# Optimization experiments

Measured on AMD Instinct MI355X. Metric: run time of the kernel, lower is better.

The kernel has to match this reference:

```python
import jax, jax.numpy as jnp
import numpy as np

B, CIN, COUT, N, TIN = 8, 64, 64, 207, 54
K, NHID, SL, KT = 8, 64, 3, 3
HEADS, STRIDE, PL = 8, 4, 8
TIME_NUM, OUT_LEN = 120, 48
E = COUT * PL            # 512 = attention embed dim (embed_size*patch_len)
PD = E // HEADS          # 64 per-head dim
PNUM = (OUT_LEN + STRIDE - PL) // STRIDE + 1   # 12 patches
EPS = 1e-5


def setup_inputs():
    keys = iter(jax.random.split(jax.random.key(0), 48))
    def rn(shape, s):
        return jax.random.normal(next(keys), shape, jnp.float32) * s
    d = {}
    d['x'] = rn((B, CIN, N, TIN), 1.0)
    d['adj'] = jax.random.uniform(next(keys), (SL, N, N), jnp.float32) / N
    d['W_conv1'] = rn((COUT, CIN), 0.125); d['b_conv1'] = rn((COUT,), 0.02)
    d['g_T'] = jnp.ones((TIN,), jnp.float32); d['b_T'] = jnp.zeros((TIN,), jnp.float32)
    d['g_S'] = jnp.ones((N,), jnp.float32); d['b_S'] = jnp.zeros((N,), jnp.float32)
    d['W_time'] = rn((2*COUT, 3*COUT, 1, KT), 1.0/np.sqrt(3*COUT*KT)); d['b_time'] = rn((2*COUT,), 0.02)
    d['wq1'] = rn((SL, K, COUT, NHID), 0.125); d['wv1'] = rn((SL, K, COUT, NHID), 0.125)
    d['bias1'] = rn((SL, NHID), 0.05)
    d['wq2'] = rn((SL, K, NHID, 2*COUT), 0.125); d['wv2'] = rn((SL, K, NHID, 2*COUT), 0.125)
    d['bias2'] = rn((SL, 2*COUT), 0.05)
    d['W_mlp'] = rn((2*COUT, SL*2*COUT, 1, KT), 1.0/np.sqrt(SL*2*COUT*KT)); d['b_mlp'] = rn((2*COUT,), 0.02)
    d['emb_T'] = rn((TIME_NUM, E), 0.02)
    d['Wq'] = rn((PD, PD), 0.125); d['bq'] = rn((PD,), 0.02)
    d['Wk'] = rn((PD, PD), 0.125); d['bk'] = rn((PD,), 0.02)
    d['Wv'] = rn((PD, PD), 0.125); d['bv'] = rn((PD,), 0.02)
    d['W_fc'] = rn((E, E), 1.0/np.sqrt(E)); d['b_fc'] = rn((E,), 0.02)
    d['g1'] = jnp.ones((E,), jnp.float32); d['b1n'] = jnp.zeros((E,), jnp.float32)
    d['g2'] = jnp.ones((E,), jnp.float32); d['b2n'] = jnp.zeros((E,), jnp.float32)
    d['W_ff1'] = rn((E, 4*COUT), 1.0/np.sqrt(E)); d['b_ff1'] = rn((4*COUT,), 0.02)
    d['W_ff2'] = rn((4*COUT, E), 1.0/np.sqrt(4*COUT)); d['b_ff2'] = rn((E,), 0.02)
    d['W_rp'] = rn((PNUM*PL, OUT_LEN), 1.0/np.sqrt(PNUM*PL)); d['b_rp'] = rn((OUT_LEN,), 0.02)
    d['g_bn'] = jnp.ones((COUT,), jnp.float32); d['b_bn'] = jnp.zeros((COUT,), jnp.float32)
    return d


def _ln(v, g, b, axis):
    m = jnp.mean(v, axis=axis, keepdims=True)
    var = jnp.var(v, axis=axis, keepdims=True)
    xhat = (v - m) * jax.lax.rsqrt(var + EPS)
    shp = [1] * v.ndim; shp[axis] = -1
    return xhat * g.reshape(shp) + b.reshape(shp)


def _gconv(x, wq, wv, bias, a):
    # x: [B,C,N,L]; wq/wv: [K,C,D]; a: [N,N]  -- multi-basis sigmoid-gated GCN
    q = jnp.einsum('bcnl,kcd->kbdnl', x, wq)
    v = jnp.einsum('bcnl,kcd->kbdnl', x, wv)
    s = jnp.sum(jax.nn.sigmoid(q) * v, axis=0)           # [B,D,N,L]
    out = jnp.einsum('nk,bcnl->bckl', a, s)              # adjacency aggregation (exact index order of source)
    return out + bias[None, :, None, None]


def _conv2d(x, w, b, dil):
    y = jax.lax.conv_general_dilated(x, w, (1, 1), 'VALID', rhs_dilation=(1, dil),
                                     dimension_numbers=('NCHW', 'OIHW', 'NCHW'))
    return y + b[None, :, None, None]


def reference(x, adj, W_conv1, b_conv1, g_T, b_T, g_S, b_S, W_time, b_time,
              wq1, wv1, bias1, wq2, wv2, bias2, W_mlp, b_mlp, emb_T,
              Wq, bq, Wk, bk, Wv, bv, W_fc, b_fc, g1, b1n, g2, b2n,
              W_ff1, b_ff1, W_ff2, b_ff2, W_rp, b_rp, g_bn, b_bn):
    residual = jnp.einsum('oc,bcnl->bonl', W_conv1, x) + b_conv1[None, :, None, None]
    xcat = jnp.concatenate([residual, _ln(residual, g_T, b_T, 3), _ln(residual, g_S, b_S, 2)], axis=1)
    h = _conv2d(xcat, W_time, b_time, 2)                 # [B,2C,N,50]
    h = jnp.tanh(h[:, :COUT]) * jax.nn.sigmoid(h[:, COUT:])
    outs = [_gconv(jax.nn.relu(_gconv(h, wq1[i], wv1[i], bias1[i], adj[i])),
                   wq2[i], wv2[i], bias2[i], adj[i]) for i in range(SL)]
    g = _conv2d(jnp.concatenate(outs, axis=1), W_mlp, b_mlp, 1)   # [B,2C,N,48]
    g = jnp.tanh(g[:, :COUT]) * jax.nn.sigmoid(g[:, COUT:])      # [B,C,N,48]
    # --- TTransformer with patching ---
    z = jnp.pad(g, ((0, 0), (0, 0), (0, 0), (0, STRIDE)))        # pad time by stride (52 >= patch_len)
    idx = jnp.arange(PNUM)[:, None] * STRIDE + jnp.arange(PL)[None, :]
    patches = z[..., idx]                                        # [B,C,N,P,PL] unfold
    q0 = patches.reshape(B, N, PNUM, E)                          # row-major reshape, as in torch source
    xe = q0 + emb_T[:PNUM][None, None]
    qh = xe.reshape(B, N, PNUM, HEADS, PD)
    qs = qh @ Wq + bq; ks = qh @ Wk + bk; vs = qh @ Wv + bv
    scores = jnp.einsum('bnqhd,bnkhd->bnqkh', qs, ks)
    att = jax.nn.softmax(scores / jnp.sqrt(jnp.float32(E)), axis=2)   # softmax over QUERY axis (faithful to source)
    ao = jnp.einsum('bnqkh,bnkhd->bnqhd', att, vs).reshape(B, N, PNUM, E) @ W_fc + b_fc
    M = _ln(ao + xe, g1, b1n, 3)
    ff = jax.nn.relu(M @ W_ff1 + b_ff1) @ W_ff2 + b_ff2
    U = _ln(M + ff, g2, b2n, 3)
    o = (U + xe + M).reshape(B, N, COUT, PNUM * PL) @ W_rp + b_rp     # [B,N,C,48]
    o = jnp.transpose(o, (0, 2, 1, 3))                               # [B,C,N,48]
    # --- BatchNorm2d (training-mode batch stats) over residual sum ---
    y = o + residual[..., -OUT_LEN:]
    m = jnp.mean(y, axis=(0, 2, 3), keepdims=True)
    var = jnp.var(y, axis=(0, 2, 3), keepdims=True)
    return (y - m) * jax.lax.rsqrt(var + EPS) * g_bn[None, :, None, None] + b_bn[None, :, None, None]
```

## Files before the change

### kernel.cpp

```cpp
#include <hip/hip_runtime.h>
#include <hip/hip_bf16.h>

#define TPB 256
#define TPA 512

constexpr int Bx = 8, Cc = 64, Nn = 207, Tin = 54, Kb = 8;
constexpr int LP = 52, NP = Nn * LP;
constexpr int NPa = 10816;
constexpr int L50 = 50, Tout = 48;
constexpr int Ee = 512, Pn = 12;
constexpr float EPSF = 1e-5f;
constexpr int SRDF = 516;

constexpr size_t O_RESID = 0;
constexpr size_t O_LNTM  = O_RESID + (size_t)Bx*Cc*Nn*Tin;
constexpr size_t O_LNTR  = O_LNTM  + (size_t)Bx*Cc*Nn;
constexpr size_t O_LNSM  = O_LNTR  + (size_t)Bx*Cc*Nn;
constexpr size_t O_LNSR  = O_LNSM  + (size_t)Bx*Cc*Tin;
constexpr size_t O_XCAT  = O_LNSR  + (size_t)Bx*Cc*Tin;
constexpr size_t O_RB    = O_XCAT  + (size_t)Bx*192*Nn*Tin;
constexpr size_t O_H     = O_RB    + (size_t)Bx*128*NP;
constexpr size_t O_GACC  = O_H     + (size_t)Bx*64*NP;
constexpr size_t O_GG    = O_GACC  + (size_t)Bx*128*Nn*Tout;
constexpr size_t O_XE    = O_GG    + (size_t)Bx*64*Nn*Tout;
constexpr size_t O_WTT   = O_XE    + (size_t)Bx*Nn*Pn*Ee;
constexpr size_t O_WTM   = O_WTT   + (size_t)128*192*3;
constexpr size_t O_BNST  = O_WTM   + (size_t)128*384*3;
constexpr size_t O_WTB   = O_BNST + 128;
constexpr size_t O_ADJT  = O_WTB  + (size_t)128*576/2;
constexpr size_t O_HT    = O_H;
constexpr size_t O_WQ1B  = O_ADJT + (size_t)3*13*7*512/2;
constexpr size_t O_WV1B  = O_WQ1B + (size_t)24*4*2*512/2;
constexpr size_t O_WQ2B  = O_WV1B + (size_t)24*4*2*512/2;
constexpr size_t O_WV2B  = O_WQ2B + (size_t)24*8*2*512/2;
constexpr size_t O_WQT   = O_WV2B + (size_t)24*8*2*512/2;
constexpr size_t O_WKT   = O_WQT  + 2048;
constexpr size_t O_WVT   = O_WKT  + 2048;
constexpr size_t O_WFCT  = O_WVT  + 2048;
constexpr size_t O_WF1T  = O_WFCT + 131072;
constexpr size_t O_WF2T  = O_WF1T + 65536;

#define FMA4(acc, sA_, vB_) { (acc).x += (sA_)*(vB_).x; (acc).y += (sA_)*(vB_).y; (acc).z += (sA_)*(vB_).z; (acc).w += (sA_)*(vB_).w; }

typedef __attribute__((ext_vector_type(8))) short bf16x8;
typedef __attribute__((ext_vector_type(4))) float f32x4;

__device__ __forceinline__ float sigm(float x){ return 1.0f/(1.0f+__expf(-x)); }
__device__ __forceinline__ ushort f2bf(float x){ __hip_bfloat16 h = __float2bfloat16(x); return *(ushort*)&h; }

__global__ __launch_bounds__(TPB) void k_residual(const float* __restrict__ x, const float* __restrict__ W,
                                                  const float* __restrict__ bias, float* __restrict__ out,
                                                  float* __restrict__ lnm, float* __restrict__ lnr){
  int n = blockIdx.x, b = blockIdx.y;
  __shared__ __align__(16) float sX[Cc][Tin];
  __shared__ __align__(16) float sW[Cc*Cc];
  __shared__ __align__(16) float sO[Cc][Tin];
  int tid = threadIdx.x;
  for(int i=tid;i<Cc*Tin;i+=TPB){ int c=i/Tin, l=i%Tin; sX[c][l] = x[((size_t)(b*Cc+c)*Nn+n)*Tin+l]; }
  for(int i=tid;i<Cc*Cc;i+=TPB) sW[i]=W[i];
  __syncthreads();
  for(int i=tid;i<Cc*Tin;i+=TPB){
    int o=i/Tin, l=i%Tin; float acc=bias[o];
    #pragma unroll 8
    for(int c=0;c<Cc;c++) acc += sW[o*Cc+c]*sX[c][l];
    out[((size_t)(b*Cc+o)*Nn+n)*Tin+l]=acc;
    sO[o][l]=acc;
  }
  __syncthreads();
  if(tid < Cc){
    float s=0.f,s2=0.f;
    for(int l=0;l<Tin;l++){ float v=sO[tid][l]; s+=v; s2+=v*v; }
    float m=s*(1.f/Tin); float var=s2*(1.f/Tin)-m*m;
    int row = (b*Cc+tid)*Nn + n;
    lnm[row]=m; lnr[row]=rsqrtf(fmaxf(var,0.f)+EPSF);
  }
}

__global__ __launch_bounds__(TPB) void k_lnS(const float* __restrict__ r, float* __restrict__ mean, float* __restrict__ rstd){
  int row = blockIdx.x*TPB + threadIdx.x;
  if(row >= Bx*Cc*Tin) return;
  int l = row % Tin; int bc = row / Tin;
  const float* p = r + (size_t)bc*Nn*Tin + l;
  float s=0.f,s2=0.f;
  for(int n=0;n<Nn;n++){ float v=p[(size_t)n*Tin]; s+=v; s2+=v*v; }
  float m=s*(1.f/Nn); float var=s2*(1.f/Nn)-m*m;
  mean[row]=m; rstd[row]=rsqrtf(fmaxf(var,0.f)+EPSF);
}

struct WJob { const float* W; ushort* F; int K, N, KS, NT, sStride, total, type; };
struct WJobs { WJob j[14]; };

__global__ __launch_bounds__(TPB) void k_wfrag_all(WJobs jobs){
  int gi = blockIdx.x*TPB + threadIdx.x;
  for(int seg=0; seg<14; seg++){
    const WJob J = jobs.j[seg];
    if(gi < J.total){
      int i = gi;
      if(J.type == 3){
        int b = i / ((NPa-NP)*64); int r = i % ((NPa-NP)*64);
        J.F[((size_t)b*NPa + NP)*64 + r] = 0;
        return;
      }
      int j = i & 7; int lane = (i>>3) & 63;
      int t = i >> 9;
      int r15 = lane & 15, hi = lane >> 4;
      float v;
      if(J.type == 0){
        int ks = t % J.KS; int r = t / J.KS; int colTile = r % J.NT; int s = r / J.NT;
        int k = ks*32 + hi*8 + j, col = colTile*16 + r15;
        v = (k < J.K && col < J.N) ? J.W[(size_t)s*J.sStride + (size_t)k*J.N + col] : 0.f;
      } else if(J.type == 1){
        int ks = t % 18; int colTile = t / 18;
        int k = ks*32 + hi*8 + j, o = colTile*16 + r15;
        int kt = k/192, ci = k - kt*192;
        v = J.W[(size_t)(o*192+ci)*3 + kt];
      } else {
        int ks = t % 12; int r = t / 12; int colTile = r & 7; int layer = r >> 3;
        int k = ks*32 + hi*8 + j;
        int kt = k >> 7, ci = k & 127;
        int o = colTile*16 + r15;
        v = J.W[(size_t)(o*384 + layer*128 + ci)*3 + kt];
      }
      J.F[i] = f2bf(v);
      return;
    }
    gi -= J.total;
  }
}

__global__ __launch_bounds__(TPB) void k_timeconv_mfma(const float* __restrict__ resid,
    const float* __restrict__ tm, const float* __restrict__ tr,
    const float* __restrict__ sm, const float* __restrict__ sr,
    const float* __restrict__ gT, const float* __restrict__ bT,
    const float* __restrict__ gS, const float* __restrict__ bS,
    const ushort* __restrict__ WF, const float* __restrict__ bias, ushort* __restrict__ HT){
  int n = blockIdx.x, b = blockIdx.y;
  constexpr int XS = 200;
  __shared__ __align__(16) ushort sXT[68*XS];
  int tid = threadIdx.x;
  for(int i=tid; i<14*XS; i+=TPB) sXT[54*XS + i] = 0;
  float gSn = gS[n], bSn = bS[n];
  for(int i=tid; i<64*54; i+=TPB){
    int cm = i/54, l = i%54;
    int rowT = (b*Cc+cm)*Nn + n;
    float r = resid[(size_t)rowT*Tin + l];
    float v1 = (r - tm[rowT]) * tr[rowT] * gT[l] + bT[l];
    int rowS = (b*Cc+cm)*Tin + l;
    float v2 = (r - sm[rowS]) * sr[rowS] * gSn + bSn;
    sXT[l*XS + cm]        = f2bf(r);
    sXT[l*XS + 64 + cm]   = f2bf(v1);
    sXT[l*XS + 128 + cm]  = f2bf(v2);
  }
  __syncthreads();
  int lane = tid & 63, w = tid >> 6;
  int r15 = lane & 15, hi = lane >> 4;
  float b0 = bias[w*16 + r15], b1 = bias[w*16 + 64 + r15];
  f32x4 acc0[4], acc1[4];
  #pragma unroll
  for(int tt=0;tt<4;tt++){
    acc0[tt][0]=b0; acc0[tt][1]=b0; acc0[tt][2]=b0; acc0[tt][3]=b0;
    acc1[tt][0]=b1; acc1[tt][1]=b1; acc1[tt][2]=b1; acc1[tt][3]=b1;
  }
  const ushort* wp0 = WF + ((size_t)w*18)*512 + lane*8;
  const ushort* wp1 = WF + ((size_t)(w+4)*18)*512 + lane*8;
  #pragma unroll 2
  for(int ks=0; ks<18; ks++){
    int k0 = ks*32 + hi*8;
    int kt = k0/192, ci0 = k0 - kt*192;
    bf16x8 bw0 = *(const bf16x8*)&wp0[(size_t)ks*512];
    bf16x8 bw1 = *(const bf16x8*)&wp1[(size_t)ks*512];
    #pragma unroll
    for(int tt=0;tt<4;tt++){
      bf16x8 ax = *(const bf16x8*)&sXT[(tt*16 + r15 + 2*kt)*XS + ci0];
      acc0[tt] = __builtin_amdgcn_mfma_f32_16x16x32_bf16(ax, bw0, acc0[tt], 0,0,0);
      acc1[tt] = __builtin_amdgcn_mfma_f32_16x16x32_bf16(ax, bw1, acc1[tt], 0,0,0);
    }
  }
  ushort* htp = HT + ((size_t)b*NPa + (size_t)n*LP)*64;
  int c = w*16 + r15;
  #pragma unroll
  for(int tt=0;tt<4;tt++){
    int t0 = tt*16 + hi*4;
    #pragma unroll
    for(int i=0;i<4;i++){
      int t = t0 + i;
      if(t < L50) htp[(size_t)t*64 + c] = f2bf(tanhf(acc0[tt][i])*sigm(acc1[tt][i]));
    }
  }
  if(tid < 128){ int cz = tid >> 1, tz = 50 + (tid & 1); htp[(size_t)tz*64 + cz] = 0; }
}

template<int D, int TR>
__global__ __launch_bounds__(TPB) void k_gcs_mfma(const ushort* __restrict__ XT,
    const ushort* __restrict__ wqF, const ushort* __restrict__ wvF,
    ushort* __restrict__ S, size_t inSlot, size_t outSlot){
  constexpr int Dt = D/16;
  constexpr int NDH = D/64;
  constexpr size_t WSTR = (size_t)Kb*Dt*2*512;
  int p0 = blockIdx.x*64;
  int b = blockIdx.z;
  int iy = blockIdx.y;
  int tid = threadIdx.x;
  int lane = tid & 63, w = tid >> 6;
  const ushort* wqB = wqF + iy*WSTR;
  const ushort* wvB = wvF + iy*WSTR;
  ushort* Sb = S + iy*outSlot;
  __shared__ __align__(16) ushort sX[64*64];
  if constexpr(TR){
    const ushort* Xp = XT + iy*inSlot;
    __shared__ __align__(16) ushort sT2[64*66];
    for(int i=tid;i<4096;i+=TPB){ int c=i>>6, col=i&63; int p=p0+col;
      sT2[c*66+col] = (p<NP) ? Xp[((size_t)(b*64+c))*NP + p] : (ushort)0; }
    __syncthreads();
    for(int i=tid;i<512;i+=TPB){
      int row=i>>3, c8=(i&7)<<3;
      ushort u[8];
      #pragma unroll
      for(int j=0;j<8;j++) u[j] = sT2[(c8+j)*66 + row];
      *(uint4*)&sX[row*64 + (c8 ^ ((row&7)<<3))] = *(uint4*)u;
    }
  } else {
    for(int i=tid;i<512;i+=TPB){
      int row=i>>3, c8=(i&7)<<3;
      uint4 v = *(const uint4*)&XT[((size_t)b*NPa + p0 + row)*64 + c8];
      *(uint4*)&sX[row*64 + (c8 ^ ((row&7)<<3))] = v;
    }
  }
  __syncthreads();
  int r15 = lane & 15, hi = lane >> 4;
  bf16x8 bf[4][2];
  #pragma unroll
  for(int pt=0;pt<4;pt++){
    int row = pt*16 + r15;
    int sw = (row&7)<<3;
    int cu0 = hi*8;
    bf[pt][0] = *(const bf16x8*)&sX[row*64 + (cu0 ^ sw)];
    bf[pt][1] = *(const bf16x8*)&sX[row*64 + ((cu0+32) ^ sw)];
  }
  #pragma unroll
  for(int dh=0; dh<NDH; dh++){
    int dTile = dh*4 + w;
    int d0 = dh*64 + (w<<4);
    f32x4 acc[4];
    #pragma unroll
    for(int pt=0;pt<4;pt++){ acc[pt][0]=0.f; acc[pt][1]=0.f; acc[pt][2]=0.f; acc[pt][3]=0.f; }
    const ushort* wqp = wqB + ((size_t)dTile*2)*512 + lane*8;
    const ushort* wvp = wvB + ((size_t)dTile*2)*512 + lane*8;
    for(int k=0;k<Kb;k++){
      bf16x8 aq0 = *(const bf16x8*)&wqp[0];
      bf16x8 aq1 = *(const bf16x8*)&wqp[512];
      bf16x8 av0 = *(const bf16x8*)&wvp[0];
      bf16x8 av1 = *(const bf16x8*)&wvp[512];
      wqp += (size_t)Dt*2*512; wvp += (size_t)Dt*2*512;
      #pragma unroll
      for(int pt=0;pt<4;pt++){
        f32x4 q; q[0]=0.f;q[1]=0.f;q[2]=0.f;q[3]=0.f;
        f32x4 v; v[0]=0.f;v[1]=0.f;v[2]=0.f;v[3]=0.f;
        q = __builtin_amdgcn_mfma_f32_16x16x32_bf16(aq0, bf[pt][0], q, 0,0,0);
        q = __builtin_amdgcn_mfma_f32_16x16x32_bf16(aq1, bf[pt][1], q, 0,0,0);
        v = __builtin_amdgcn_mfma_f32_16x16x32_bf16(av0, bf[pt][0], v, 0,0,0);
        v = __builtin_amdgcn_mfma_f32_16x16x32_bf16(av1, bf[pt][1], v, 0,0,0);
        #pragma unroll
        for(int i=0;i<4;i++) acc[pt][i] += v[i]*sigm(q[i]);
      }
    }
    #pragma unroll
    for(int pt=0;pt<4;pt++){
      int p = p0 + pt*16 + r15;
      if(p < NP){
        #pragma unroll
        for(int i=0;i<4;i++){
          int d = d0 + hi*4 + i;
          Sb[((size_t)b*D + d)*NP + p] = f2bf(acc[pt][i]);
        }
      }
    }
  }
}

template<int RELU>
__global__ __launch_bounds__(TPB) void k_agg_mfma(const ushort* __restrict__ S, const ushort* __restrict__ adjF,
                                                  const float* __restrict__ bias,
                                                  ushort* __restrict__ O0, ushort* __restrict__ O1, ushort* __restrict__ O2,
                                                  int D, size_t inSlot){
  int d = blockIdx.x;
  int by = blockIdx.y;
  int b = by / 3, li = by % 3;
  int bd = b*D + d;
  const ushort* adjL = adjF + (size_t)li*13*7*512;
  constexpr int SST = 232;
  __shared__ __align__(16) ushort sB[64*SST];
  int tid = threadIdx.x;
  for(int i=tid*8; i<64*SST; i+=TPB*8){ uint4 z; z.x=0;z.y=0;z.z=0;z.w=0; *(uint4*)&sB[i]=z; }
  __syncthreads();
  const ushort* Sp = S + li*inSlot + (size_t)bd*NP;
  for(int i=tid; i<NP; i+=TPB){
    int nn = i/52, l = i - nn*52;
    sB[l*SST + nn] = Sp[i];
  }
  __syncthreads();
  int lane = tid & 63, w = tid >> 6;
  int r15 = lane & 15, hi = lane >> 4;
  float bb = bias[li*D + d];
  ushort* Ob = (li==0) ? O0 : (li==1 ? O1 : O2);
  ushort* Op = Ob + (size_t)bd*NP;
  for(int k2t = w; k2t < 13; k2t += 4){
    f32x4 acc[4];
    #pragma unroll
    for(int lt=0;lt<4;lt++){ acc[lt][0]=0;acc[lt][1]=0;acc[lt][2]=0;acc[lt][3]=0; }
    #pragma unroll
    for(int ks=0; ks<7; ks++){
      bf16x8 a = *(const bf16x8*)&adjL[((size_t)(k2t*7 + ks))*512 + lane*8];
      #pragma unroll
      for(int lt=0;lt<4;lt++){
        bf16x8 bfr = *(const bf16x8*)&sB[(lt*16+r15)*SST + ks*32 + hi*8];
        acc[lt] = __builtin_amdgcn_mfma_f32_16x16x32_bf16(a, bfr, acc[lt], 0,0,0);
      }
    }
    #pragma unroll
    for(int lt=0;lt<4;lt++){
      #pragma unroll
      for(int i2=0;i2<4;i2++){
        int k2 = k2t*16 + hi*4 + i2;
        int l  = lt*16 + r15;
        if(k2 < Nn && l < LP){
          float v = acc[lt][i2] + bb;
          if(RELU) v = fmaxf(v, 0.f);
          Op[(size_t)k2*LP + l] = f2bf(v);
        }
      }
    }
  }
}

__global__ __launch_bounds__(TPB) void k_mlp_all(const ushort* __restrict__ RB0, const ushort* __restrict__ RB1,
                                                 const ushort* __restrict__ RB2, const ushort* __restrict__ WF,
                                                 const float* __restrict__ bm, const float* __restrict__ emb,
                                                 float* __restrict__ xe){
  int n = blockIdx.x, b = blockIdx.y;
  constexpr int CS = 136;
  __shared__ __align__(16) ushort sLT[3*52*CS];
  int tid = threadIdx.x;
  {
    const ushort* Rp = RB0;
    for(int i=tid;i<6656;i+=TPB){ int c=i/52, l=i%52; sLT[0*52*CS + l*CS + c] = Rp[(((size_t)b*128+c)*Nn + n)*LP + l]; }
    Rp = RB1;
    for(int i=tid;i<6656;i+=TPB){ int c=i/52, l=i%52; sLT[1*52*CS + l*CS + c] = Rp[(((size_t)b*128+c)*Nn + n)*LP + l]; }
    Rp = RB2;
    for(int i=tid;i<6656;i+=TPB){ int c=i/52, l=i%52; sLT[2*52*CS + l*CS + c] = Rp[(((size_t)b*128+c)*Nn + n)*LP + l]; }
  }
  __syncthreads();
  int lane = tid & 63, w = tid >> 6;
  int r15 = lane & 15, hi = lane >> 4;
  f32x4 acc0[3], acc1[3];
  #pragma unroll
  for(int tt=0;tt<3;tt++){
    acc0[tt][0]=0;acc0[tt][1]=0;acc0[tt][2]=0;acc0[tt][3]=0;
    acc1[tt][0]=0;acc1[tt][1]=0;acc1[tt][2]=0;acc1[tt][3]=0;
  }
  #pragma unroll
  for(int layer=0; layer<3; layer++){
    const ushort* wp0 = WF + ((size_t)(layer*8 + w)*12)*512 + lane*8;
    const ushort* wp1 = WF + ((size_t)(layer*8 + w+4)*12)*512 + lane*8;
    const ushort* sL = &sLT[layer*52*CS];
    #pragma unroll 3
    for(int ks=0; ks<12; ks++){
      int kt = ks>>2, ci0 = (ks&3)*32 + hi*8;
      bf16x8 bw0 = *(const bf16x8*)&wp0[(size_t)ks*512];
      bf16x8 bw1 = *(const bf16x8*)&wp1[(size_t)ks*512];
      #pragma unroll
      for(int tt=0;tt<3;tt++){
        bf16x8 ax = *(const bf16x8*)&sL[(tt*16 + r15 + kt)*CS + ci0];
        acc0[tt] = __builtin_amdgcn_mfma_f32_16x16x32_bf16(ax, bw0, acc0[tt], 0,0,0);
        acc1[tt] = __builtin_amdgcn_mfma_f32_16x16x32_bf16(ax, bw1, acc1[tt], 0,0,0);
      }
    }
  }
  int o = w*16 + r15;
  float b0 = bm[o], b1 = bm[o+64];
  float* xeb = xe + (size_t)b*1271808;
  int off0 = o*19872 + n*96;
  #pragma unroll
  for(int tt=0;tt<3;tt++){
    #pragma unroll
    for(int i2=0;i2<4;i2++){
      int tq = tt*16 + hi*4 + i2;
      float v = tanhf(acc0[tt][i2] + b0)*sigm(acc1[tt][i2] + b1);
      int p1 = tq>>2, j1 = tq&3;
      int offa = off0 + p1*8 + j1;
      xeb[offa] = v + emb[(size_t)((offa>>9)%12)*Ee + (offa&511)];
      if(tq >= 4){
        int offb = off0 + (p1-1)*8 + j1 + 4;
        xeb[offb] = v + emb[(size_t)((offb>>9)%12)*Ee + (offb&511)];
      }
    }
  }
  {
    int o2 = tid >> 2, r2 = 92 + (tid & 3);
    int offp = o2*19872 + n*96 + r2;
    xeb[offp] = emb[(size_t)((offp>>9)%12)*Ee + (offp&511)];
  }
}

template<int NW>
__device__ __forceinline__ void ln_rows(float* buf, const float* __restrict__ g, const float* __restrict__ be, int tid){
  int lane = tid & 63, wv = tid >> 6;
  for(int r = wv; r < 12; r += NW){
    float s=0.f, s2=0.f;
    #pragma unroll
    for(int j=0;j<8;j++){ float v = buf[r*SRDF + j*64 + lane]; s+=v; s2+=v*v; }
    #pragma unroll
    for(int off=32; off; off>>=1){ s += __shfl_xor(s,off); s2 += __shfl_xor(s2,off); }
    float m = s*(1.f/512.f);
    float rstd = rsqrtf(fmaxf(s2*(1.f/512.f)-m*m, 0.f)+EPSF);
    #pragma unroll
    for(int j=0;j<8;j++){ int e = j*64+lane; float v = buf[r*SRDF+e];
      buf[r*SRDF+e] = (v-m)*rstd*g[e] + be[e]; }
  }
}

__global__ __launch_bounds__(TPA,2) void k_attn(
    const float* __restrict__ xe, const float* __restrict__ resid,
    const ushort* __restrict__ WqF, const float* __restrict__ bq,
    const ushort* __restrict__ WkF, const float* __restrict__ bk,
    const ushort* __restrict__ WvF, const float* __restrict__ bv,
    const ushort* __restrict__ WfcF, const float* __restrict__ bfc,
    const float* __restrict__ g1, const float* __restrict__ b1n,
    const float* __restrict__ g2, const float* __restrict__ b2n,
    const ushort* __restrict__ Wff1F, const float* __restrict__ bff1,
    const ushort* __restrict__ Wff2F, const float* __restrict__ bff2,
    const float* __restrict__ Wrp, const float* __restrict__ brp,
    float* __restrict__ y)
{
  int n = blockIdx.x, b = blockIdx.y;
  __shared__ __align__(16) ushort SbX[16*512];
  __shared__ __align__(16) ushort Mb[16*256];
  __shared__ __align__(16) float U0[12*SRDF];
  __shared__ __align__(16) float U1[12*SRDF];
  __shared__ __align__(16) float sS[1160];
  int tid = threadIdx.x;
  int lane = tid & 63, w = tid >> 6;
  int r15 = lane & 15, hi = lane >> 4;
  const float* __restrict__ xeg = xe + ((size_t)b*Nn + n)*6144;

  for(int i=tid;i<1024;i+=TPA){
    int r = i>>6, ch = i&63;
    ushort u[8];
    if(r<12){
      const float* s = &xeg[r*512 + ch*8];
      #pragma unroll
      for(int j=0;j<8;j++) u[j] = f2bf(s[j]);
    } else {
      #pragma unroll
      for(int j=0;j<8;j++) u[j] = 0;
    }
    *(uint4*)&SbX[r*512 + ((ch ^ (r&7))<<3)] = *(uint4*)u;
  }
  for(int i=tid;i<128;i+=TPA){
    int r = 12 + (i>>5), ch = i&31;
    uint4 z; z.x=0;z.y=0;z.z=0;z.w=0;
    *(uint4*)&Mb[r*256 + ch*8] = z;
  }
  __syncthreads();

  f32x4 vfrag[4];
  {
    int head = w;
    bf16x8 a0, a1;
    { int ch0 = head*8 + hi, ch1 = head*8 + 4 + hi;
      a0 = *(const bf16x8*)&SbX[r15*512 + ((ch0 ^ (r15&7))<<3)];
      a1 = *(const bf16x8*)&SbX[r15*512 + ((ch1 ^ (r15&7))<<3)]; }
    #pragma unroll
    for(int nt=0;nt<4;nt++){
      int col = nt*16 + r15;
      float bb = bq[col];
      f32x4 acc; acc[0]=bb;acc[1]=bb;acc[2]=bb;acc[3]=bb;
      acc = __builtin_amdgcn_mfma_f32_16x16x32_bf16(a0, *(const bf16x8*)&WqF[(size_t)(nt*2+0)*512 + lane*8], acc, 0,0,0);
      acc = __builtin_amdgcn_mfma_f32_16x16x32_bf16(a1, *(const bf16x8*)&WqF[(size_t)(nt*2+1)*512 + lane*8], acc, 0,0,0);
      #pragma unroll
      for(int i2=0;i2<4;i2++){ int p = hi*4+i2; if(p<12) U0[p*SRDF + head*64 + col] = acc[i2]; }
    }
    #pragma unroll
    for(int nt=0;nt<4;nt++){
      int col = nt*16 + r15;
      float bb = bk[col];
      f32x4 acc; acc[0]=bb;acc[1]=bb;acc[2]=bb;acc[3]=bb;
      acc = __builtin_amdgcn_mfma_f32_16x16x32_bf16(a0, *(const bf16x8*)&WkF[(size_t)(nt*2+0)*512 + lane*8], acc, 0,0,0);
      acc = __builtin_amdgcn_mfma_f32_16x16x32_bf16(a1, *(const bf16x8*)&WkF[(size_t)(nt*2+1)*512 + lane*8], acc, 0,0,0);
      #pragma unroll
      for(int i2=0;i2<4;i2++){ int p = hi*4+i2; if(p<12) U1[p*SRDF + head*64 + col] = acc[i2]; }
    }
    #pragma unroll
    for(int nt=0;nt<4;nt++){
      int col = nt*16 + r15;
      float bb = bv[col];
      f32x4 acc; acc[0]=bb;acc[1]=bb;acc[2]=bb;acc[3]=bb;
      acc = __builtin_amdgcn_mfma_f32_16x16x32_bf16(a0, *(const bf16x8*)&WvF[(size_t)(nt*2+0)*512 + lane*8], acc, 0,0,0);
      acc = __builtin_amdgcn_mfma_f32_16x16x32_bf16(a1, *(const bf16x8*)&WvF[(size_t)(nt*2+1)*512 + lane*8], acc, 0,0,0);
      vfrag[nt] = acc;
    }
  }
  __syncthreads();

  const float scale = 0.04419417382415922f;
  for(int i=tid;i<1152;i+=TPA){
    int q = i%12, kh = i/12; int h2 = kh&7, k2 = kh>>3;
    const float* qp = &U0[q*SRDF + h2*64];
    const float* kp = &U1[k2*SRDF + h2*64];
    float s=0.f;
    #pragma unroll
    for(int d4=0; d4<16; d4++){
      float4 a4 = *(const float4*)&qp[d4*4];
      float4 b4 = *(const float4*)&kp[d4*4];
      s += a4.x*b4.x + a4.y*b4.y + a4.z*b4.z + a4.w*b4.w;
    }
    sS[i] = s*scale;
  }
  __syncthreads();
  {
    int head = w;
    #pragma unroll
    for(int nt=0;nt<4;nt++){
      int col = nt*16 + r15;
      #pragma unroll
      for(int i2=0;i2<4;i2++){ int p = hi*4+i2; if(p<12) U0[p*SRDF + head*64 + col] = vfrag[nt][i2]; }
    }
  }
  if(tid<96){
    float mx=-1e30f;
    for(int q=0;q<12;q++) mx = fmaxf(mx, sS[tid*12+q]);
    float sm=0.f;
    for(int q=0;q<12;q++){ float e = __expf(sS[tid*12+q]-mx); sS[tid*12+q]=e; sm+=e; }
    float inv = 1.f/sm;
    for(int q=0;q<12;q++) sS[tid*12+q] *= inv;
  }
  __syncthreads();

  for(int i=tid;i<6144;i+=TPA){
    int q=i>>9, h2=(i>>6)&7, d=i&63;
    float s=0.f;
    #pragma unroll
    for(int k2=0;k2<12;k2++) s += sS[(k2*8+h2)*12+q]*U0[k2*SRDF+h2*64+d];
    int kk = i & 511;
    SbX[q*512 + (((kk>>3) ^ (q&7))<<3) + (kk&7)] = f2bf(s);
  }
  __syncthreads();

  {
    f32x4 acc[4];
    #pragma unroll
    for(int nt=0;nt<4;nt++){ float bb = bfc[(w*4+nt)*16 + r15]; acc[nt][0]=bb;acc[nt][1]=bb;acc[nt][2]=bb;acc[nt][3]=bb; }
    for(int ks=0;ks<16;ks++){
      int ch = ks*4 + hi;
      bf16x8 a = *(const bf16x8*)&SbX[r15*512 + ((ch ^ (r15&7))<<3)];
      #pragma unroll
      for(int nt=0;nt<4;nt++){
        acc[nt] = __builtin_amdgcn_mfma_f32_16x16x32_bf16(a, *(const bf16x8*)&WfcF[(size_t)((w*4+nt)*16 + ks)*512 + lane*8], acc[nt], 0,0,0);
      }
    }
    #pragma unroll
    for(int nt=0;nt<4;nt++){
      int col = (w*4+nt)*16 + r15;
      #pragma unroll
      for(int i2=0;i2<4;i2++){ int p = hi*4+i2; if(p<12) U1[p*SRDF + col] = acc[nt][i2] + xeg[p*512 + col]; }
    }
  }
  __syncthreads();
  ln_rows<8>(U1, g1, b1n, tid);
  __syncthreads();

  for(int i=tid;i<6144;i+=TPA){
    int r=i>>9, kk=i&511;
    SbX[r*512 + (((kk>>3) ^ (r&7))<<3) + (kk&7)] = f2bf(U1[r*SRDF + kk]);
  }
  __syncthreads();

  {
    f32x4 acc[2];
    #pragma unroll
    for(int nt=0;nt<2;nt++){ float bb = bff1[(w*2+nt)*16 + r15]; acc[nt][0]=bb;acc[nt][1]=bb;acc[nt][2]=bb;acc[nt][3]=bb; }
    for(int ks=0;ks<16;ks++){
      int ch = ks*4 + hi;
      bf16x8 a = *(const bf16x8*)&SbX[r15*512 + ((ch ^ (r15&7))<<3)];
      #pragma unroll
      for(int nt=0;nt<2;nt++){
        acc[nt] = __builtin_amdgcn_mfma_f32_16x16x32_bf16(a, *(const bf16x8*)&Wff1F[(size_t)((w*2+nt)*16 + ks)*512 + lane*8], acc[nt], 0,0,0);
      }
    }
    #pragma unroll
    for(int nt=0;nt<2;nt++){
      int u = (w*2+nt)*16 + r15;
      #pragma unroll
      for(int i2=0;i2<4;i2++){
        int p = hi*4+i2;
        if(p<12) Mb[p*256 + (((u>>3) ^ (p&7))<<3) + (u&7)] = f2bf(fmaxf(acc[nt][i2], 0.f));
      }
    }
  }
  __syncthreads();

  {
    f32x4 acc[4];
    #pragma unroll
    for(int nt=0;nt<4;nt++){ float bb = bff2[(w*4+nt)*16 + r15]; acc[nt][0]=bb;acc[nt][1]=bb;acc[nt][2]=bb;acc[nt][3]=bb; }
    for(int ks=0;ks<8;ks++){
      int ch = ks*4 + hi;
      bf16x8 a = *(const bf16x8*)&Mb[r15*256 + ((ch ^ (r15&7))<<3)];
      #pragma unroll
      for(int nt=0;nt<4;nt++){
        acc[nt] = __builtin_amdgcn_mfma_f32_16x16x32_bf16(a, *(const bf16x8*)&Wff2F[(size_t)((w*4+nt)*8 + ks)*512 + lane*8], acc[nt], 0,0,0);
      }
    }
    #pragma unroll
    for(int nt=0;nt<4;nt++){
      int col = (w*4+nt)*16 + r15;
      #pragma unroll
      for(int i2=0;i2<4;i2++){ int p = hi*4+i2; if(p<12) U0[p*SRDF + col] = acc[nt][i2] + U1[p*SRDF + col]; }
    }
  }
  __syncthreads();
  ln_rows<8>(U0, g2, b2n, tid);
  __syncthreads();

  for(int i=tid;i<6144;i+=TPA){
    int r=i>>9, c=i&511;
    U1[r*SRDF+c] = U0[r*SRDF+c] + U1[r*SRDF+c] + xeg[r*512+c];
  }
  __syncthreads();
  for(int i=tid;i<4608;i+=TPA) U0[i] = Wrp[i];
  __syncthreads();
  #pragma unroll
  for(int j=0;j<2;j++){
    int i4 = tid + j*TPA;
    if(i4 < 768){
      int c = i4/12, tq = i4%12; int t0 = tq*4;
      float4 acc = *(const float4*)&brp[t0];
      for(int t96=0;t96<96;t96++){
        int f = c*96 + t96;
        float a = U1[(f>>9)*SRDF + (f&511)];
        float4 w4 = *(const float4*)&U0[t96*48 + t0];
        FMA4(acc, a, w4);
      }
      size_t rb = (((size_t)b*Cc+c)*Nn + n)*Tin + 6 + t0;
      acc.x += resid[rb+0]; acc.y += resid[rb+1]; acc.z += resid[rb+2]; acc.w += resid[rb+3];
      *(float4*)&y[(((size_t)b*Cc+c)*Nn + n)*Tout + t0] = acc;
    }
  }
}

__global__ __launch_bounds__(TPB) void k_bnstats(const float* __restrict__ y, float* __restrict__ stats){
  int c = blockIdx.x; int tid = threadIdx.x;
  float s=0.f,s2=0.f;
  const int per = Nn*Tout;
  for(int idx=tid; idx<Bx*per; idx+=TPB){
    int b = idx/per, r = idx%per;
    float v = y[((size_t)b*Cc+c)*per + r];
    s+=v; s2+=v*v;
  }
  __shared__ float rs[TPB], rs2[TPB];
  rs[tid]=s; rs2[tid]=s2; __syncthreads();
  for(int off=TPB/2; off; off>>=1){ if(tid<off){ rs[tid]+=rs[tid+off]; rs2[tid]+=rs2[tid+off]; } __syncthreads(); }
  if(tid==0){
    float m = rs[0]/(float)(Bx*per);
    float var = rs2[0]/(float)(Bx*per) - m*m;
    stats[c]=m; stats[64+c]=rsqrtf(fmaxf(var,0.f)+EPSF);
  }
}
__global__ __launch_bounds__(TPB) void k_bnout(const float* __restrict__ y, const float* __restrict__ stats,
                                               const float* __restrict__ gbn, const float* __restrict__ bbn,
                                               float* __restrict__ out){
  size_t i = (size_t)blockIdx.x*TPB + threadIdx.x;
  if(i >= (size_t)Bx*Cc*Nn*Tout) return;
  int c = (int)((i/(Nn*Tout))%Cc);
  out[i] = (y[i]-stats[c])*stats[64+c]*gbn[c] + bbn[c];
}

extern "C" void kernel_launch(void* const* d_in, const int* in_sizes, int n_in,
                              void* d_out, int out_size, void* d_ws, size_t ws_size,
                              hipStream_t stream) {
  const float* x      = (const float*)d_in[0];
  const float* adj    = (const float*)d_in[1];
  const float* Wconv1 = (const float*)d_in[2];
  const float* bconv1 = (const float*)d_in[3];
  const float* gT     = (const float*)d_in[4];
  const float* bT     = (const float*)d_in[5];
  const float* gS     = (const float*)d_in[6];
  const float* bS     = (const float*)d_in[7];
  const float* Wtime  = (const float*)d_in[8];
  const float* btime  = (const float*)d_in[9];
  const float* wq1    = (const float*)d_in[10];
  const float* wv1    = (const float*)d_in[11];
  const float* bias1  = (const float*)d_in[12];
  const float* wq2    = (const float*)d_in[13];
  const float* wv2    = (const float*)d_in[14];
  const float* bias2  = (const float*)d_in[15];
  const float* Wmlp   = (const float*)d_in[16];
  const float* bmlp   = (const float*)d_in[17];
  const float* embT   = (const float*)d_in[18];
  const float* Wq     = (const float*)d_in[19];
  const float* bq     = (const float*)d_in[20];
  const float* Wk     = (const float*)d_in[21];
  const float* bk     = (const float*)d_in[22];
  const float* Wv     = (const float*)d_in[23];
  const float* bv     = (const float*)d_in[24];
  const float* Wfc    = (const float*)d_in[25];
  const float* bfc    = (const float*)d_in[26];
  const float* g1     = (const float*)d_in[27];
  const float* b1n    = (const float*)d_in[28];
  const float* g2     = (const float*)d_in[29];
  const float* b2n    = (const float*)d_in[30];
  const float* Wff1   = (const float*)d_in[31];
  const float* bff1   = (const float*)d_in[32];
  const float* Wff2   = (const float*)d_in[33];
  const float* bff2   = (const float*)d_in[34];
  const float* Wrp    = (const float*)d_in[35];
  const float* brp    = (const float*)d_in[36];
  const float* gbn    = (const float*)d_in[37];
  const float* bbn    = (const float*)d_in[38];

  float* ws = (float*)d_ws;
  float* RESID = ws + O_RESID;
  float* LNTM  = ws + O_LNTM;
  float* LNTR  = ws + O_LNTR;
  float* LNSM  = ws + O_LNSM;
  float* LNSR  = ws + O_LNSR;
  const size_t RSLOT  = (size_t)Bx*128*NP;
  const size_t S1SLOT = (size_t)Bx*64*NP;
  ushort* RAx  = (ushort*)(ws + O_XCAT);
  ushort* RB0  = (ushort*)(ws + O_RB);
  ushort* RB1  = RB0 + RSLOT;
  ushort* RB2  = (ushort*)(ws + O_GACC);
  ushort* S1x  = (ushort*)(ws + O_GACC);
  float* Y     = ws + O_GG;
  float* XE    = ws + O_XE;
  float* BNST  = ws + O_BNST;
  ushort* WTMF = (ushort*)(ws + O_WTM);
  ushort* WTB  = (ushort*)(ws + O_WTB);
  ushort* ADJT = (ushort*)(ws + O_ADJT);
  ushort* HT   = (ushort*)(ws + O_HT);
  ushort* WQ1B = (ushort*)(ws + O_WQ1B);
  ushort* WV1B = (ushort*)(ws + O_WV1B);
  ushort* WQ2B = (ushort*)(ws + O_WQ2B);
  ushort* WV2B = (ushort*)(ws + O_WV2B);
  ushort* WQT  = (ushort*)(ws + O_WQT);
  ushort* WKT  = (ushort*)(ws + O_WKT);
  ushort* WVT  = (ushort*)(ws + O_WVT);
  ushort* WFCT = (ushort*)(ws + O_WFCT);
  ushort* WF1T = (ushort*)(ws + O_WF1T);
  ushort* WF2T = (ushort*)(ws + O_WF2T);

  k_residual<<<dim3(Nn,Bx),TPB,0,stream>>>(x, Wconv1, bconv1, RESID, LNTM, LNTR);
  k_lnS<<<(Bx*Cc*Tin)/TPB,TPB,0,stream>>>(RESID, LNSM, LNSR);

  WJobs jobs;
  jobs.j[0]  = { wq1,  WQ1B, 64,  64,  2,  4,  64*64,   24*4*2*512, 0 };
  jobs.j[1]  = { wv1,  WV1B, 64,  64,  2,  4,  64*64,   24*4*2*512, 0 };
  jobs.j[2]  = { wq2,  WQ2B, 64,  128, 2,  8,  64*128,  24*8*2*512, 0 };
  jobs.j[3]  = { wv2,  WV2B, 64,  128, 2,  8,  64*128,  24*8*2*512, 0 };
  jobs.j[4]  = { Wq,   WQT,  64,  64,  2,  4,  64*64,   4*2*512,    0 };
  jobs.j[5]  = { Wk,   WKT,  64,  64,  2,  4,  64*64,   4*2*512,    0 };
  jobs.j[6]  = { Wv,   WVT,  64,  64,  2,  4,  64*64,   4*2*512,    0 };
  jobs.j[7]  = { Wfc,  WFCT, 512, 512, 16, 32, 512*512, 32*16*512,  0 };
  jobs.j[8]  = { Wff1, WF1T, 512, 256, 16, 16, 512*256, 16*16*512,  0 };
  jobs.j[9]  = { Wff2, WF2T, 256, 512, 8,  32, 256*512, 32*8*512,   0 };
  jobs.j[10] = { adj,  ADJT, 207, 207, 7,  13, Nn*Nn,   3*13*7*512, 0 };
  jobs.j[11] = { Wtime, WTB, 0,   0,   0,  0,  0,       8*18*512,   1 };
  jobs.j[12] = { Wmlp, WTMF, 0,   0,   0,  0,  0,       3*8*12*512, 2 };
  jobs.j[13] = { nullptr, HT, 0,  0,   0,  0,  0,       Bx*(NPa-NP)*64, 3 };
  int totalW = 2*(24*4*2*512) + 2*(24*8*2*512) + 3*(4*2*512) + 32*16*512 + 16*16*512 + 32*8*512
             + 3*13*7*512 + 8*18*512 + 3*8*12*512 + Bx*(NPa-NP)*64;
  k_wfrag_all<<<(totalW+TPB-1)/TPB,TPB,0,stream>>>(jobs);

  k_timeconv_mfma<<<dim3(Nn,Bx),TPB,0,stream>>>(RESID, LNTM, LNTR, LNSM, LNSR, gT, bT, gS, bS,
                                                WTB, btime, HT);

  k_gcs_mfma<64,0><<<dim3(169,3,Bx),TPB,0,stream>>>(HT, WQ1B, WV1B, RAx, 0, RSLOT);
  k_agg_mfma<1><<<dim3(64,Bx*3),TPB,0,stream>>>(RAx, ADJT, bias1, S1x, S1x+S1SLOT, S1x+2*S1SLOT, 64, RSLOT);
  k_gcs_mfma<128,1><<<dim3(169,3,Bx),TPB,0,stream>>>(S1x, WQ2B, WV2B, RAx, S1SLOT, RSLOT);
  k_agg_mfma<0><<<dim3(128,Bx*3),TPB,0,stream>>>(RAx, ADJT, bias2, RB0, RB1, RB2, 128, RSLOT);
  k_mlp_all<<<dim3(Nn,Bx),TPB,0,stream>>>(RB0, RB1, RB2, WTMF, bmlp, embT, XE);
  k_attn<<<dim3(Nn,Bx),TPA,0,stream>>>(XE, RESID, WQT,bq, WKT,bk, WVT,bv, WFCT,bfc,
                                       g1,b1n,g2,b2n, WF1T,bff1, WF2T,bff2, Wrp,brp, Y);
  k_bnstats<<<64,TPB,0,stream>>>(Y, BNST);
  k_bnout<<<(Bx*Cc*Nn*Tout)/TPB,TPB,0,stream>>>(Y, BNST, gbn, bbn, (float*)d_out);
}
```

Baseline: 792.6 us.

## Fuse spatial LN stats into residual via atomics and split BN stats reduction

Removes the separate k_lnS kernel by accumulating per-(b,c,l) sums and squared sums with atomicAdd inside k_residual; timeconv derives mean/rstd from them. BN stats reduction is split into 16 chunks per channel with atomic accumulation, and k_bnout computes mean/rstd itself. This removes a strided re-read and raises parallelism of the BN reduction, at the cost of many contended float atomics, two memsets, and E[x^2]-m^2 numerics with nondeterministic summation order.

```diff
diff --git a/kernel.cpp b/kernel.cpp
--- a/kernel.cpp
+++ b/kernel.cpp
@@ -50,7 +50,8 @@
 
 __global__ __launch_bounds__(TPB) void k_residual(const float* __restrict__ x, const float* __restrict__ W,
                                                   const float* __restrict__ bias, float* __restrict__ out,
-                                                  float* __restrict__ lnm, float* __restrict__ lnr){
+                                                  float* __restrict__ lnm, float* __restrict__ lnr,
+                                                  float* __restrict__ lnsS, float* __restrict__ lnsS2){
   int n = blockIdx.x, b = blockIdx.y;
   __shared__ __align__(16) float sX[Cc][Tin];
   __shared__ __align__(16) float sW[Cc*Cc];
@@ -74,17 +75,13 @@
     int row = (b*Cc+tid)*Nn + n;
     lnm[row]=m; lnr[row]=rsqrtf(fmaxf(var,0.f)+EPSF);
   }
-}
-
-__global__ __launch_bounds__(TPB) void k_lnS(const float* __restrict__ r, float* __restrict__ mean, float* __restrict__ rstd){
-  int row = blockIdx.x*TPB + threadIdx.x;
-  if(row >= Bx*Cc*Tin) return;
-  int l = row % Tin; int bc = row / Tin;
-  const float* p = r + (size_t)bc*Nn*Tin + l;
-  float s=0.f,s2=0.f;
-  for(int n=0;n<Nn;n++){ float v=p[(size_t)n*Tin]; s+=v; s2+=v*v; }
-  float m=s*(1.f/Nn); float var=s2*(1.f/Nn)-m*m;
-  mean[row]=m; rstd[row]=rsqrtf(fmaxf(var,0.f)+EPSF);
+  for(int i=tid;i<Cc*Tin;i+=TPB){
+    int c=i/Tin, l=i%Tin;
+    float v = sO[c][l];
+    int row = (b*Cc+c)*Tin + l;
+    atomicAdd(&lnsS[row], v);
+    atomicAdd(&lnsS2[row], v*v);
+  }
 }
 
 struct WJob { const float* W; ushort* F; int K, N, KS, NT, sStride, total, type; };
@@ -130,7 +127,7 @@
 
 __global__ __launch_bounds__(TPB) void k_timeconv_mfma(const float* __restrict__ resid,
     const float* __restrict__ tm, const float* __restrict__ tr,
-    const float* __restrict__ sm, const float* __restrict__ sr,
+    const float* __restrict__ lnsS, const float* __restrict__ lnsS2,
     const float* __restrict__ gT, const float* __restrict__ bT,
     const float* __restrict__ gS, const float* __restrict__ bS,
     const ushort* __restrict__ WF, const float* __restrict__ bias, ushort* __restrict__ HT){
@@ -146,7 +143,9 @@
     float r = resid[(size_t)rowT*Tin + l];
     float v1 = (r - tm[rowT]) * tr[rowT] * gT[l] + bT[l];
     int rowS = (b*Cc+cm)*Tin + l;
-    float v2 = (r - sm[rowS]) * sr[rowS] * gSn + bSn;
+    float sm_ = lnsS[rowS]*(1.f/Nn);
+    float sr_ = rsqrtf(fmaxf(lnsS2[rowS]*(1.f/Nn) - sm_*sm_, 0.f)+EPSF);
+    float v2 = (r - sm_) * sr_ * gSn + bSn;
     sXT[l*XS + cm]        = f2bf(r);
     sXT[l*XS + 64 + cm]   = f2bf(v1);
     sXT[l*XS + 128 + cm]  = f2bf(v2);
@@ -649,10 +648,12 @@
 }
 
 __global__ __launch_bounds__(TPB) void k_bnstats(const float* __restrict__ y, float* __restrict__ stats){
-  int c = blockIdx.x; int tid = threadIdx.x;
+  int c = blockIdx.x; int chunk = blockIdx.y; int tid = threadIdx.x;
+  const int per = Nn*Tout;
+  const int total = Bx*per;
+  const int CH = total/16;
   float s=0.f,s2=0.f;
-  const int per = Nn*Tout;
-  for(int idx=tid; idx<Bx*per; idx+=TPB){
+  for(int idx=chunk*CH+tid; idx<chunk*CH+CH; idx+=TPB){
     int b = idx/per, r = idx%per;
     float v = y[((size_t)b*Cc+c)*per + r];
     s+=v; s2+=v*v;
@@ -661,9 +662,8 @@
   rs[tid]=s; rs2[tid]=s2; __syncthreads();
   for(int off=TPB/2; off; off>>=1){ if(tid<off){ rs[tid]+=rs[tid+off]; rs2[tid]+=rs2[tid+off]; } __syncthreads(); }
   if(tid==0){
-    float m = rs[0]/(float)(Bx*per);
-    float var = rs2[0]/(float)(Bx*per) - m*m;
-    stats[c]=m; stats[64+c]=rsqrtf(fmaxf(var,0.f)+EPSF);
+    atomicAdd(&stats[c], rs[0]);
+    atomicAdd(&stats[64+c], rs2[0]);
   }
 }
 __global__ __launch_bounds__(TPB) void k_bnout(const float* __restrict__ y, const float* __restrict__ stats,
@@ -672,7 +672,11 @@
   size_t i = (size_t)blockIdx.x*TPB + threadIdx.x;
   if(i >= (size_t)Bx*Cc*Nn*Tout) return;
   int c = (int)((i/(Nn*Tout))%Cc);
-  out[i] = (y[i]-stats[c])*stats[64+c]*gbn[c] + bbn[c];
+  const float cnt = (float)(Bx*Nn*Tout);
+  float m = stats[c]/cnt;
+  float var = stats[64+c]/cnt - m*m;
+  float rstd = rsqrtf(fmaxf(var,0.f)+EPSF);
+  out[i] = (y[i]-m)*rstd*gbn[c] + bbn[c];
 }
 
 extern "C" void kernel_launch(void* const* d_in, const int* in_sizes, int n_in,
@@ -722,8 +726,8 @@
   float* RESID = ws + O_RESID;
   float* LNTM  = ws + O_LNTM;
   float* LNTR  = ws + O_LNTR;
-  float* LNSM  = ws + O_LNSM;
-  float* LNSR  = ws + O_LNSR;
+  float* LNSS  = ws + O_LNSM;
+  float* LNSS2 = ws + O_LNSR;
   const size_t RSLOT  = (size_t)Bx*128*NP;
   const size_t S1SLOT = (size_t)Bx*64*NP;
   ushort* RAx  = (ushort*)(ws + O_XCAT);
@@ -749,8 +753,10 @@
   ushort* WF1T = (ushort*)(ws + O_WF1T);
   ushort* WF2T = (ushort*)(ws + O_WF2T);
 
-  k_residual<<<dim3(Nn,Bx),TPB,0,stream>>>(x, Wconv1, bconv1, RESID, LNTM, LNTR);
-  k_lnS<<<(Bx*Cc*Tin)/TPB,TPB,0,stream>>>(RESID, LNSM, LNSR);
+  hipMemsetAsync(LNSS, 0, (size_t)2*Bx*Cc*Tin*sizeof(float), stream);
+  hipMemsetAsync(BNST, 0, 128*sizeof(float), stream);
+
+  k_residual<<<dim3(Nn,Bx),TPB,0,stream>>>(x, Wconv1, bconv1, RESID, LNTM, LNTR, LNSS, LNSS2);
 
   WJobs jobs;
   jobs.j[0]  = { wq1,  WQ1B, 64,  64,  2,  4,  64*64,   24*4*2*512, 0 };
@@ -771,7 +777,7 @@
              + 3*13*7*512 + 8*18*512 + 3*8*12*512 + Bx*(NPa-NP)*64;
   k_wfrag_all<<<(totalW+TPB-1)/TPB,TPB,0,stream>>>(jobs);
 
-  k_timeconv_mfma<<<dim3(Nn,Bx),TPB,0,stream>>>(RESID, LNTM, LNTR, LNSM, LNSR, gT, bT, gS, bS,
+  k_timeconv_mfma<<<dim3(Nn,Bx),TPB,0,stream>>>(RESID, LNTM, LNTR, LNSS, LNSS2, gT, bT, gS, bS,
                                                 WTB, btime, HT);
 
   k_gcs_mfma<64,0><<<dim3(169,3,Bx),TPB,0,stream>>>(HT, WQ1B, WV1B, RAx, 0, RSLOT);
@@ -781,6 +787,6 @@
   k_mlp_all<<<dim3(Nn,Bx),TPB,0,stream>>>(RB0, RB1, RB2, WTMF, bmlp, embT, XE);
   k_attn<<<dim3(Nn,Bx),TPA,0,stream>>>(XE, RESID, WQT,bq, WKT,bk, WVT,bv, WFCT,bfc,
                                        g1,b1n,g2,b2n, WF1T,bff1, WF2T,bff2, Wrp,brp, Y);
-  k_bnstats<<<64,TPB,0,stream>>>(Y, BNST);
+  k_bnstats<<<dim3(64,16),TPB,0,stream>>>(Y, BNST);
   k_bnout<<<(Bx*Cc*Nn*Tout)/TPB,TPB,0,stream>>>(Y, BNST, gbn, bbn, (float*)d_out);
 }
```

After: 737.2 us. -7.0%, faster.
